# Kernel tuning notes

Measured on AMD Instinct MI355X. Metric: run time of the kernel, lower is better.

The kernel has to match this reference:

```python
import jax, jax.numpy as jnp
import numpy as np

NUM_HEADS = 8
LN_EPS = 1e-5


def setup_inputs() -> dict:
    key = jax.random.key(0)
    ks = jax.random.split(key, 8)
    B, H, W, C = 2, 64, 64, 256
    return {
        "x": jax.random.normal(ks[0], (B, H, W, C), dtype=jnp.float32),
        "cond": jax.random.normal(ks[1], (B, C), dtype=jnp.float32),
        "t": jax.random.randint(ks[2], (B,), 0, 100, dtype=jnp.int64),
        "emb_table": jax.random.normal(ks[3], (100, C), dtype=jnp.float32) * 0.02,
        "ada_w": jax.random.normal(ks[4], (C, 2 * C), dtype=jnp.float32) * 0.02,
        "ada_b": jnp.zeros((2 * C,), dtype=jnp.float32),
        "qkv_w": jax.random.normal(ks[5], (C, 3 * C), dtype=jnp.float32) * 0.02,
        "qkv_b": jnp.zeros((3 * C,), dtype=jnp.float32),
        "proj_w": jax.random.normal(ks[6], (C, C), dtype=jnp.float32) * 0.02,
        "proj_b": jnp.zeros((C,), dtype=jnp.float32),
    }


def reference(x, cond, t, emb_table, ada_w, ada_b, qkv_w, qkv_b, proj_w, proj_b):
    B, H, W, C = x.shape
    N = H * W
    h = NUM_HEADS
    d = C // h
    scale = d ** -0.5

    x = x.reshape(B, N, C)

    # AdaLayerNorm (adalayernorm_abs): timestep embedding -> SiLU -> Linear -> scale/shift
    emb = emb_table[t]                                # [B, C]
    ss = jax.nn.silu(emb) @ ada_w + ada_b             # [B, 2C]
    sc, sh = jnp.split(ss, 2, axis=-1)                # each [B, C]
    mu = jnp.mean(x, axis=-1, keepdims=True)
    var = jnp.var(x, axis=-1, keepdims=True)
    xn = (x - mu) * jax.lax.rsqrt(var + LN_EPS)       # LN without affine
    x = xn * (1.0 + sc[:, None, :]) + sh[:, None, :]

    # QKV projection and head split
    qkv = (x @ qkv_w + qkv_b).reshape(B, N, 3, h, d)
    qkv = jnp.transpose(qkv, (2, 0, 3, 1, 4))          # [3, B, h, N, d]
    q, k, v = qkv[0], qkv[1], qkv[2]

    # Manual attention: full [B, h, N, N] scores (matches original module)
    attn = jnp.einsum('bhnd,bhmd->bhnm', q, k) * scale
    attn = jax.nn.softmax(attn, axis=-1)
    out = jnp.einsum('bhnm,bhmd->bhnd', attn, v)       # [B, h, N, d]
    out = jnp.transpose(out, (0, 2, 1, 3)).reshape(B, N, C)

    out = (out.reshape(B, H, W, C) @ proj_w) + proj_b
    return out
```

## Files before the change

### kernel.cpp

```cpp
#include <hip/hip_runtime.h>
#include <hip/hip_bf16.h>
#include <stdint.h>

typedef __attribute__((ext_vector_type(8))) short bfrag;
typedef __attribute__((ext_vector_type(4))) short bfrag4;
typedef __attribute__((ext_vector_type(4))) float f32x4;
typedef __attribute__((ext_vector_type(2))) float f32x2;
typedef __attribute__((ext_vector_type(2))) unsigned int u32x2;

__device__ inline short f2bf(float f) {
  union { float f; uint32_t u; } v; v.f = f;
  uint32_t u = v.u;
  uint32_t r = (u + 0x7fffu + ((u >> 16) & 1u)) >> 16;
  return (short)r;
}
__device__ inline float bf2f(short s) {
  return __builtin_bit_cast(float, (uint32_t)((uint32_t)(uint16_t)s << 16));
}

#if __has_builtin(__builtin_amdgcn_cvt_pk_bf16_f32)
typedef __attribute__((ext_vector_type(2))) __bf16 bf16x2_t;
__device__ inline uint32_t pack_bf16(float a, float b) {
  bf16x2_t r = __builtin_amdgcn_cvt_pk_bf16_f32(a, b);
  return __builtin_bit_cast(uint32_t, r);
}
#else
__device__ inline uint32_t pack_bf16(float a, float b) {
  uint32_t ua = __builtin_bit_cast(uint32_t, a) + 0x8000u;
  uint32_t ub = __builtin_bit_cast(uint32_t, b) + 0x8000u;
  return __builtin_amdgcn_perm(ub, ua, 0x07060302);
}
#endif

__global__ __launch_bounds__(256) void prep_kernel(
    const float* __restrict__ emb_table, const int* __restrict__ t,
    const float* __restrict__ ada_w, const float* __restrict__ ada_b,
    float* __restrict__ scsh,
    const float* __restrict__ qkv_w, short* __restrict__ qkv_wt,
    const float* __restrict__ proj_w, short* __restrict__ proj_wt) {
  __shared__ float smem[64 * 65];
  const int blk = blockIdx.x;
  const int tid = threadIdx.x;
  if (blk < 16) {
    float* se = smem;
    float* part = smem + 256;
    int b = blk >> 3, ox = blk & 7;
    int tt = t[b];
    float e = emb_table[tt * 256 + tid];
    se[tid] = e / (1.f + __expf(-e));
    __syncthreads();
    int ol = tid & 63, kc = tid >> 6;
    int o = ox * 64 + ol;
    float acc = 0.f;
#pragma unroll 8
    for (int k = kc * 64; k < (kc + 1) * 64; ++k) acc += se[k] * ada_w[k * 512 + o];
    part[tid] = acc;
    __syncthreads();
    if (tid < 64) {
      int oo = ox * 64 + tid;
      scsh[b * 512 + oo] =
          part[tid] + part[64 + tid] + part[128 + tid] + part[192 + tid] + ada_b[oo];
    }
  } else {
    const float* W; short* Wt; int N, lb;
    if (blk < 64) { W = qkv_w; Wt = qkv_wt; N = 768; lb = blk - 16; }
    else          { W = proj_w; Wt = proj_wt; N = 256; lb = blk - 64; }
    float (*tile)[65] = (float(*)[65])smem;
    int k0 = (lb & 3) * 64, n0 = (lb >> 2) * 64;
    int r = tid >> 2, c0 = (tid & 3) * 16;
    const float* src = W + (long)(k0 + r) * N + n0 + c0;
#pragma unroll
    for (int j = 0; j < 16; j += 4) {
      float4 v = *(const float4*)(src + j);
      tile[r][c0 + j] = v.x; tile[r][c0 + j + 1] = v.y;
      tile[r][c0 + j + 2] = v.z; tile[r][c0 + j + 3] = v.w;
    }
    __syncthreads();
    int nl = tid >> 2, kc = (tid & 3) * 16;
    short outv[16];
#pragma unroll
    for (int j = 0; j < 16; ++j) outv[j] = f2bf(tile[kc + j][nl]);
    short* dst = Wt + (long)(n0 + nl) * 256 + k0 + kc;
    *(bfrag*)dst = *(bfrag*)&outv[0];
    *(bfrag*)(dst + 8) = *(bfrag*)&outv[8];
  }
}

__global__ __launch_bounds__(256) void ln_kernel(const float* __restrict__ x,
                                                 const float* __restrict__ scsh,
                                                 short* __restrict__ xb) {
  int row = blockIdx.x * 4 + (threadIdx.x >> 6);
  int b = row >> 12;
  int lane = threadIdx.x & 63;
  float4 v = *(const float4*)(x + (long)row * 256 + lane * 4);
  float s = v.x + v.y + v.z + v.w;
  float sq = v.x * v.x + v.y * v.y + v.z * v.z + v.w * v.w;
#pragma unroll
  for (int off = 32; off > 0; off >>= 1) {
    s += __shfl_xor(s, off);
    sq += __shfl_xor(sq, off);
  }
  float mu = s * (1.f / 256.f);
  float var = sq * (1.f / 256.f) - mu * mu;
  float rstd = rsqrtf(var + 1e-5f);
  const float* scp = scsh + b * 512 + lane * 4;
  float4 sc = *(const float4*)scp;
  float4 sh = *(const float4*)(scp + 256);
  float y0 = (v.x - mu) * rstd * (1.f + sc.x) + sh.x;
  float y1 = (v.y - mu) * rstd * (1.f + sc.y) + sh.y;
  float y2 = (v.z - mu) * rstd * (1.f + sc.z) + sh.z;
  float y3 = (v.w - mu) * rstd * (1.f + sc.w) + sh.w;
  u32x2 o; o.x = pack_bf16(y0, y1); o.y = pack_bf16(y2, y3);
  *(u32x2*)&xb[(long)row * 256 + lane * 4] = o;
}

__global__ __launch_bounds__(256) void gemm_qkv(const short* __restrict__ A,
                                                const short* __restrict__ Bt,
                                                const float* __restrict__ bias,
                                                float qscale,
                                                short* __restrict__ qk,
                                                short* __restrict__ vT) {
  __shared__ short As[128 * 40];
  __shared__ short Bs[64 * 40];
  const int mt = blockIdx.x, nt = blockIdx.y;
  const int tid = threadIdx.x;
  const int w = tid >> 6, lane = tid & 63, l16 = lane & 15, quad = lane >> 4;
  const int ar = tid >> 1, ak = (tid & 1) * 16;
  const int br = tid >> 2, bk = (tid & 3) * 8;
  f32x4 acc[2][4] = {};
  const short* Arow = A + (long)(mt * 128 + ar) * 256 + ak;
  const short* Brow = Bt + (long)(nt * 64 + br) * 256 + bk;
  bfrag a8a = *(const bfrag*)Arow;
  bfrag a8b = *(const bfrag*)(Arow + 8);
  bfrag b8  = *(const bfrag*)Brow;
  for (int kk = 0; kk < 8; ++kk) {
    __syncthreads();
    *(bfrag*)&As[ar * 40 + ak] = a8a;
    *(bfrag*)&As[ar * 40 + ak + 8] = a8b;
    *(bfrag*)&Bs[br * 40 + bk] = b8;
    __syncthreads();
    int kn = (kk < 7) ? (kk + 1) : 7;
    a8a = *(const bfrag*)(Arow + kn * 32);
    a8b = *(const bfrag*)(Arow + kn * 32 + 8);
    b8  = *(const bfrag*)(Brow + kn * 32);
    bfrag a0 = *(const bfrag*)&As[(w * 32 + l16) * 40 + quad * 8];
    bfrag a1 = *(const bfrag*)&As[(w * 32 + 16 + l16) * 40 + quad * 8];
#pragma unroll
    for (int c = 0; c < 4; ++c) {
      bfrag bf = *(const bfrag*)&Bs[(c * 16 + l16) * 40 + quad * 8];
      acc[0][c] = __builtin_amdgcn_mfma_f32_16x16x32_bf16(a0, bf, acc[0][c], 0, 0, 0);
      acc[1][c] = __builtin_amdgcn_mfma_f32_16x16x32_bf16(a1, bf, acc[1][c], 0, 0, 0);
    }
  }
  const int rowb = mt * 128 + w * 32 + quad * 4;
  if (nt < 8) {
#pragma unroll
    for (int rg = 0; rg < 2; ++rg) {
      int row0 = rowb + rg * 16;
#pragma unroll
      for (int c = 0; c < 4; ++c) {
        int col = nt * 64 + c * 16 + l16;
        float bv = bias[col];
        float mult = (col < 256) ? qscale : 1.0f;
#pragma unroll
        for (int r = 0; r < 4; ++r)
          qk[(long)(row0 + r) * 512 + col] = f2bf((acc[rg][c][r] + bv) * mult);
      }
    }
  } else {
    const int bb = mt >> 5;
#pragma unroll
    for (int rg = 0; rg < 2; ++rg) {
      int keyl = (rowb + rg * 16) & 4095;
#pragma unroll
      for (int c = 0; c < 4; ++c) {
        int col = nt * 64 + c * 16 + l16;
        float bv = bias[col];
        int d = col - 512;
        u32x2 dd;
        dd.x = pack_bf16(acc[rg][c][0] + bv, acc[rg][c][1] + bv);
        dd.y = pack_bf16(acc[rg][c][2] + bv, acc[rg][c][3] + bv);
        *(u32x2*)&vT[((long)(bb * 8 + (d >> 5)) * 32 + (d & 31)) * 4096 + keyl] = dd;
      }
    }
  }
}

__global__ __launch_bounds__(256) void attn_kernel(const short* __restrict__ qk,
                                                   const short* __restrict__ vT,
                                                   short* __restrict__ OpB,
                                                   float* __restrict__ lpart) {
  const int blk = blockIdx.x;
  const int qt = blk & 31;
  const int bh = (blk >> 5) & 15;
  const int ks = blk >> 9;
  const int b = bh >> 3, hh = bh & 7;
  const int tid = threadIdx.x;
  const int w = tid >> 6, lane = tid & 63, l16 = lane & 15, quad = lane >> 4;

  __shared__ short Ks[2][64 * 40];
  __shared__ short Vt[2][32 * 68];

  const long rowbase = (long)b * 4096;
  const int qrow0 = qt * 128 + w * 32 + l16;
  bfrag qf[2];
#pragma unroll
  for (int g = 0; g < 2; ++g)
    qf[g] = *(const bfrag*)&qk[(rowbase + qrow0 + g * 16) * 512 + hh * 32 + quad * 8];

  f32x4 o0[2] = {}, o1[2] = {};
  f32x2 lsum[2] = {};

  const int si = tid >> 2, sk = (tid & 3) * 8;
  const int vrow = tid >> 3, vcol = (tid & 7) * 8;
  const short* ksrc = qk + rowbase * 512 + 256 + hh * 32 + (long)si * 512 + sk;
  const short* vsrc = vT + ((long)bh * 32 + vrow) * 4096 + vcol;

  const int kt0 = ks * 16;
  bfrag k8 = *(const bfrag*)(ksrc + (long)kt0 * 64 * 512);
  bfrag v8 = *(const bfrag*)(vsrc + kt0 * 64);

  int buf = 0;
  for (int i = 0; i < 16; ++i) {
    *(bfrag*)&Ks[buf][si * 40 + sk] = k8;
    *(bfrag*)&Vt[buf][vrow * 68 + vcol] = v8;
    __syncthreads();
    int nn = (i < 15) ? (i + 1) : 15;
    k8 = *(const bfrag*)(ksrc + (long)(kt0 + nn) * 64 * 512);
    v8 = *(const bfrag*)(vsrc + (kt0 + nn) * 64);

#pragma unroll
    for (int nt = 0; nt < 4; ++nt) {
      bfrag kf = *(const bfrag*)&Ks[buf][(nt * 16 + l16) * 40 + quad * 8];
      f32x4 z = {0, 0, 0, 0};
      f32x4 s[2];
      __builtin_amdgcn_s_setprio(1);
      s[0] = __builtin_amdgcn_mfma_f32_16x16x32_bf16(kf, qf[0], z, 0, 0, 0);
      s[1] = __builtin_amdgcn_mfma_f32_16x16x32_bf16(kf, qf[1], z, 0, 0, 0);
      __builtin_amdgcn_s_setprio(0);
      bfrag4 pb[2];
#pragma unroll
      for (int g = 0; g < 2; ++g) {
        float p0 = __builtin_amdgcn_exp2f(s[g][0]);
        float p1 = __builtin_amdgcn_exp2f(s[g][1]);
        float p2 = __builtin_amdgcn_exp2f(s[g][2]);
        float p3 = __builtin_amdgcn_exp2f(s[g][3]);
        f32x2 pa = {p0, p1}, pc = {p2, p3};
        lsum[g] += pa; lsum[g] += pc;
        u32x2 pk; pk.x = pack_bf16(p0, p1); pk.y = pack_bf16(p2, p3);
        pb[g] = __builtin_bit_cast(bfrag4, pk);
      }
      bfrag4 va = *(const bfrag4*)&Vt[buf][l16 * 68 + nt * 16 + quad * 4];
      bfrag4 vb = *(const bfrag4*)&Vt[buf][(16 + l16) * 68 + nt * 16 + quad * 4];
      __builtin_amdgcn_s_setprio(1);
#pragma unroll
      for (int g = 0; g < 2; ++g) {
        o0[g] = __builtin_amdgcn_mfma_f32_16x16x16bf16_1k(va, pb[g], o0[g], 0, 0, 0);
        o1[g] = __builtin_amdgcn_mfma_f32_16x16x16bf16_1k(vb, pb[g], o1[g], 0, 0, 0);
      }
      __builtin_amdgcn_s_setprio(0);
    }
    buf ^= 1;
  }
#pragma unroll
  for (int g = 0; g < 2; ++g) {
    float ls = lsum[g].x + lsum[g].y;
    ls += __shfl_xor(ls, 16); ls += __shfl_xor(ls, 32);
    const long pbase = (((long)ks * 16 + bh) * 4096 + qrow0 + g * 16) * 32;
    u32x2 dA, dB;
    dA.x = pack_bf16(o0[g][0], o0[g][1]); dA.y = pack_bf16(o0[g][2], o0[g][3]);
    dB.x = pack_bf16(o1[g][0], o1[g][1]); dB.y = pack_bf16(o1[g][2], o1[g][3]);
    *(u32x2*)&OpB[pbase + quad * 4] = dA;
    *(u32x2*)&OpB[pbase + 16 + quad * 4] = dB;
    if (quad == 0)
      lpart[((long)ks * 16 + bh) * 4096 + qrow0 + g * 16] = ls;
  }
}

__global__ __launch_bounds__(256) void proj_kernel(const short* __restrict__ OpB,
                                                   const float* __restrict__ lpart,
                                                   const short* __restrict__ Bt,
                                                   const float* __restrict__ bias,
                                                   float* __restrict__ out) {
  __shared__ short As[128 * 40];
  __shared__ short Bs[64 * 40];
  const int mt = blockIdx.x, nt = blockIdx.y;
  const int tid = threadIdx.x;
  const int w = tid >> 6, lane = tid & 63, l16 = lane & 15, quad = lane >> 4;
  const int ar = tid >> 1, ak = (tid & 1) * 16;
  const int br = tid >> 2, bk = (tid & 3) * 8;
  f32x4 acc[2][4] = {};

  const int row = mt * 128 + ar;
  const int q = row & 4095, bq = row >> 12;
  const short* Brow = Bt + (long)(nt * 64 + br) * 256 + bk;

  long lb0 = (long)(bq * 8) * 4096 + q;
  bfrag pa[4][2];
  f32x4 pl;
#pragma unroll
  for (int ks = 0; ks < 4; ++ks) {
    long base = (lb0 + (long)ks * 16 * 4096) * 32 + ak;
    pa[ks][0] = *(const bfrag*)&OpB[base];
    pa[ks][1] = *(const bfrag*)&OpB[base + 8];
    pl[ks] = lpart[lb0 + (long)ks * 16 * 4096];
  }
  bfrag b8 = *(const bfrag*)Brow;

  for (int kk = 0; kk < 8; ++kk) {
    float linv = 1.f / (pl[0] + pl[1] + pl[2] + pl[3]);
    short av[16];
#pragma unroll
    for (int h = 0; h < 2; ++h) {
#pragma unroll
      for (int j = 0; j < 8; j += 2) {
        float v0 = (bf2f(pa[0][h][j]) + bf2f(pa[1][h][j]) +
                    bf2f(pa[2][h][j]) + bf2f(pa[3][h][j])) * linv;
        float v1 = (bf2f(pa[0][h][j+1]) + bf2f(pa[1][h][j+1]) +
                    bf2f(pa[2][h][j+1]) + bf2f(pa[3][h][j+1])) * linv;
        *(uint32_t*)&av[h * 8 + j] = pack_bf16(v0, v1);
      }
    }
    __syncthreads();
    *(bfrag*)&As[ar * 40 + ak] = *(bfrag*)&av[0];
    *(bfrag*)&As[ar * 40 + ak + 8] = *(bfrag*)&av[8];
    *(bfrag*)&Bs[br * 40 + bk] = b8;
    __syncthreads();
    int kn = (kk < 7) ? (kk + 1) : 7;
    long lbn = (long)(bq * 8 + kn) * 4096 + q;
#pragma unroll
    for (int ks = 0; ks < 4; ++ks) {
      long base = (lbn + (long)ks * 16 * 4096) * 32 + ak;
      pa[ks][0] = *(const bfrag*)&OpB[base];
      pa[ks][1] = *(const bfrag*)&OpB[base + 8];
      pl[ks] = lpart[lbn + (long)ks * 16 * 4096];
    }
    b8 = *(const bfrag*)(Brow + kn * 32);

    bfrag a0 = *(const bfrag*)&As[(w * 32 + l16) * 40 + quad * 8];
    bfrag a1 = *(const bfrag*)&As[(w * 32 + 16 + l16) * 40 + quad * 8];
#pragma unroll
    for (int c = 0; c < 4; ++c) {
      bfrag bf = *(const bfrag*)&Bs[(c * 16 + l16) * 40 + quad * 8];
      acc[0][c] = __builtin_amdgcn_mfma_f32_16x16x32_bf16(a0, bf, acc[0][c], 0, 0, 0);
      acc[1][c] = __builtin_amdgcn_mfma_f32_16x16x32_bf16(a1, bf, acc[1][c], 0, 0, 0);
    }
  }
  const int rowb = mt * 128 + w * 32 + quad * 4;
#pragma unroll
  for (int rg = 0; rg < 2; ++rg) {
    int row0 = rowb + rg * 16;
#pragma unroll
    for (int c = 0; c < 4; ++c) {
      int col = nt * 64 + c * 16 + l16;
      float bv = bias[col];
#pragma unroll
      for (int r = 0; r < 4; ++r)
        out[(long)(row0 + r) * 256 + col] = acc[rg][c][r] + bv;
    }
  }
}

extern "C" void kernel_launch(void* const* d_in, const int* in_sizes, int n_in,
                              void* d_out, int out_size, void* d_ws, size_t ws_size,
                              hipStream_t stream) {
  const float* x      = (const float*)d_in[0];
  const int*   t      = (const int*)d_in[2];
  const float* emb    = (const float*)d_in[3];
  const float* ada_w  = (const float*)d_in[4];
  const float* ada_b  = (const float*)d_in[5];
  const float* qkv_w  = (const float*)d_in[6];
  const float* qkv_b  = (const float*)d_in[7];
  const float* proj_w = (const float*)d_in[8];
  const float* proj_b = (const float*)d_in[9];

  char* ws = (char*)d_ws;
  float* scsh     = (float*)(ws);
  short* qkv_wt   = (short*)(ws + 4096);
  short* proj_wt  = (short*)(ws + 397312);
  short* xb       = (short*)(ws + 528384);
  short* qk_out   = (short*)(ws + 4722688);
  short* vT       = (short*)(ws + 13111296);
  short* OpB      = (short*)(ws + 21499904);
  float* lpart    = (float*)(ws + 38277120);

  const float QS = 0.17677669529663687f * 1.4426950408889634f;

  prep_kernel<<<80, 256, 0, stream>>>(emb, t, ada_w, ada_b, scsh,
                                      qkv_w, qkv_wt, proj_w, proj_wt);
  ln_kernel<<<2048, 256, 0, stream>>>(x, scsh, xb);
  gemm_qkv<<<dim3(64, 12), 256, 0, stream>>>(xb, qkv_wt, qkv_b, QS, qk_out, vT);
  attn_kernel<<<2048, 256, 0, stream>>>(qk_out, vT, OpB, lpart);
  proj_kernel<<<dim3(64, 4), 256, 0, stream>>>(OpB, lpart, proj_wt, proj_b,
                                               (float*)d_out);
}
```

Baseline: 165.9 us.

## Drop split-K attention; each block processes all keys and normalizes in-kernel

```diff
diff --git a/kernel.cpp b/kernel.cpp
--- a/kernel.cpp
+++ b/kernel.cpp
@@ -188,12 +188,11 @@
 
 __global__ __launch_bounds__(256) void attn_kernel(const short* __restrict__ qk,
                                                    const short* __restrict__ vT,
-                                                   short* __restrict__ OpB,
-                                                   float* __restrict__ lpart) {
-  const int blk = blockIdx.x;
+                                                   short* __restrict__ OpB) {
+  const int bid = blockIdx.x;
+  const int blk = (bid & 7) * 64 + (bid >> 3);
   const int qt = blk & 31;
-  const int bh = (blk >> 5) & 15;
-  const int ks = blk >> 9;
+  const int bh = blk >> 5;
   const int b = bh >> 3, hh = bh & 7;
   const int tid = threadIdx.x;
   const int w = tid >> 6, lane = tid & 63, l16 = lane & 15, quad = lane >> 4;
@@ -216,18 +215,17 @@
   const short* ksrc = qk + rowbase * 512 + 256 + hh * 32 + (long)si * 512 + sk;
   const short* vsrc = vT + ((long)bh * 32 + vrow) * 4096 + vcol;
 
-  const int kt0 = ks * 16;
-  bfrag k8 = *(const bfrag*)(ksrc + (long)kt0 * 64 * 512);
-  bfrag v8 = *(const bfrag*)(vsrc + kt0 * 64);
+  bfrag k8 = *(const bfrag*)ksrc;
+  bfrag v8 = *(const bfrag*)vsrc;
 
   int buf = 0;
-  for (int i = 0; i < 16; ++i) {
+  for (int i = 0; i < 64; ++i) {
     *(bfrag*)&Ks[buf][si * 40 + sk] = k8;
     *(bfrag*)&Vt[buf][vrow * 68 + vcol] = v8;
     __syncthreads();
-    int nn = (i < 15) ? (i + 1) : 15;
-    k8 = *(const bfrag*)(ksrc + (long)(kt0 + nn) * 64 * 512);
-    v8 = *(const bfrag*)(vsrc + (kt0 + nn) * 64);
+    int nn = (i < 63) ? (i + 1) : 63;
+    k8 = *(const bfrag*)(ksrc + (long)nn * 64 * 512);
+    v8 = *(const bfrag*)(vsrc + nn * 64);
 
 #pragma unroll
     for (int nt = 0; nt < 4; ++nt) {
@@ -266,19 +264,19 @@
   for (int g = 0; g < 2; ++g) {
     float ls = lsum[g].x + lsum[g].y;
     ls += __shfl_xor(ls, 16); ls += __shfl_xor(ls, 32);
-    const long pbase = (((long)ks * 16 + bh) * 4096 + qrow0 + g * 16) * 32;
+    float inv = __builtin_amdgcn_rcpf(ls);
+    const long pbase = ((long)bh * 4096 + qrow0 + g * 16) * 32;
     u32x2 dA, dB;
-    dA.x = pack_bf16(o0[g][0], o0[g][1]); dA.y = pack_bf16(o0[g][2], o0[g][3]);
-    dB.x = pack_bf16(o1[g][0], o1[g][1]); dB.y = pack_bf16(o1[g][2], o1[g][3]);
+    dA.x = pack_bf16(o0[g][0] * inv, o0[g][1] * inv);
+    dA.y = pack_bf16(o0[g][2] * inv, o0[g][3] * inv);
+    dB.x = pack_bf16(o1[g][0] * inv, o1[g][1] * inv);
+    dB.y = pack_bf16(o1[g][2] * inv, o1[g][3] * inv);
     *(u32x2*)&OpB[pbase + quad * 4] = dA;
     *(u32x2*)&OpB[pbase + 16 + quad * 4] = dB;
-    if (quad == 0)
-      lpart[((long)ks * 16 + bh) * 4096 + qrow0 + g * 16] = ls;
   }
 }
 
 __global__ __launch_bounds__(256) void proj_kernel(const short* __restrict__ OpB,
-                                                   const float* __restrict__ lpart,
                                                    const short* __restrict__ Bt,
                                                    const float* __restrict__ bias,
                                                    float* __restrict__ out) {
@@ -294,48 +292,22 @@
   const int row = mt * 128 + ar;
   const int q = row & 4095, bq = row >> 12;
   const short* Brow = Bt + (long)(nt * 64 + br) * 256 + bk;
-
-  long lb0 = (long)(bq * 8) * 4096 + q;
-  bfrag pa[4][2];
-  f32x4 pl;
-#pragma unroll
-  for (int ks = 0; ks < 4; ++ks) {
-    long base = (lb0 + (long)ks * 16 * 4096) * 32 + ak;
-    pa[ks][0] = *(const bfrag*)&OpB[base];
-    pa[ks][1] = *(const bfrag*)&OpB[base + 8];
-    pl[ks] = lpart[lb0 + (long)ks * 16 * 4096];
-  }
-  bfrag b8 = *(const bfrag*)Brow;
+  const short* Abase = OpB + ((long)(bq * 8) * 4096 + q) * 32 + ak;
+
+  bfrag a8a = *(const bfrag*)Abase;
+  bfrag a8b = *(const bfrag*)(Abase + 8);
+  bfrag b8  = *(const bfrag*)Brow;
 
   for (int kk = 0; kk < 8; ++kk) {
-    float linv = 1.f / (pl[0] + pl[1] + pl[2] + pl[3]);
-    short av[16];
-#pragma unroll
-    for (int h = 0; h < 2; ++h) {
-#pragma unroll
-      for (int j = 0; j < 8; j += 2) {
-        float v0 = (bf2f(pa[0][h][j]) + bf2f(pa[1][h][j]) +
-                    bf2f(pa[2][h][j]) + bf2f(pa[3][h][j])) * linv;
-        float v1 = (bf2f(pa[0][h][j+1]) + bf2f(pa[1][h][j+1]) +
-                    bf2f(pa[2][h][j+1]) + bf2f(pa[3][h][j+1])) * linv;
-        *(uint32_t*)&av[h * 8 + j] = pack_bf16(v0, v1);
-      }
-    }
-    __syncthreads();
-    *(bfrag*)&As[ar * 40 + ak] = *(bfrag*)&av[0];
-    *(bfrag*)&As[ar * 40 + ak + 8] = *(bfrag*)&av[8];
+    __syncthreads();
+    *(bfrag*)&As[ar * 40 + ak] = a8a;
+    *(bfrag*)&As[ar * 40 + ak + 8] = a8b;
     *(bfrag*)&Bs[br * 40 + bk] = b8;
     __syncthreads();
     int kn = (kk < 7) ? (kk + 1) : 7;
-    long lbn = (long)(bq * 8 + kn) * 4096 + q;
-#pragma unroll
-    for (int ks = 0; ks < 4; ++ks) {
-      long base = (lbn + (long)ks * 16 * 4096) * 32 + ak;
-      pa[ks][0] = *(const bfrag*)&OpB[base];
-      pa[ks][1] = *(const bfrag*)&OpB[base + 8];
-      pl[ks] = lpart[lbn + (long)ks * 16 * 4096];
-    }
-    b8 = *(const bfrag*)(Brow + kn * 32);
+    a8a = *(const bfrag*)(Abase + (long)kn * 4096 * 32);
+    a8b = *(const bfrag*)(Abase + (long)kn * 4096 * 32 + 8);
+    b8  = *(const bfrag*)(Brow + kn * 32);
 
     bfrag a0 = *(const bfrag*)&As[(w * 32 + l16) * 40 + quad * 8];
     bfrag a1 = *(const bfrag*)&As[(w * 32 + 16 + l16) * 40 + quad * 8];
@@ -382,7 +354,6 @@
   short* qk_out   = (short*)(ws + 4722688);
   short* vT       = (short*)(ws + 13111296);
   short* OpB      = (short*)(ws + 21499904);
-  float* lpart    = (float*)(ws + 38277120);
 
   const float QS = 0.17677669529663687f * 1.4426950408889634f;
 
@@ -390,7 +361,7 @@
                                       qkv_w, qkv_wt, proj_w, proj_wt);
   ln_kernel<<<2048, 256, 0, stream>>>(x, scsh, xb);
   gemm_qkv<<<dim3(64, 12), 256, 0, stream>>>(xb, qkv_wt, qkv_b, QS, qk_out, vT);
-  attn_kernel<<<2048, 256, 0, stream>>>(qk_out, vT, OpB, lpart);
-  proj_kernel<<<dim3(64, 4), 256, 0, stream>>>(OpB, lpart, proj_wt, proj_b,
+  attn_kernel<<<512, 256, 0, stream>>>(qk_out, vT, OpB);
+  proj_kernel<<<dim3(64, 4), 256, 0, stream>>>(OpB, proj_wt, proj_b,
                                                (float*)d_out);
 }
```

New measurement: 178.4 us. 1.08x slower.
